# Performance work log

Measured on AMD Instinct MI355X. Metric: run time of the kernel, lower is better.

## Reference

```python
import jax, jax.numpy as jnp
import numpy as np
from jax import lax

B, C, P = 8, 32, 256      # batch, channels, patch side
KB = 2                    # buf_region = kernel_size - stride = 3 - 1
R_MASK = 1                # output_bypassing: last-column patch, r = small_padding = 1


def setup_inputs() -> dict:
    key = jax.random.key(0)
    ks = jax.random.split(key, 5)
    x = jax.random.normal(ks[0], (B, C, P, P), jnp.float32)
    # right-halo stored by the left-neighbor patch (store_right -> last 2 cols)
    rbuf = jax.random.normal(ks[1], (B, C, P, KB), jnp.float32)
    # bottom-halo stored by the top-neighbor patch AFTER its hcat (width P+2)
    bbuf = jax.random.normal(ks[2], (B, C, KB, P + KB), jnp.float32)
    W = jax.random.normal(ks[3], (C, C, 3, 3), jnp.float32) * 0.05
    bias = jax.random.normal(ks[4], (C,), jnp.float32) * 0.05
    return {"x": x, "rbuf": rbuf, "bbuf": bbuf, "W": W, "bias": bias}


def reference(x, rbuf, bbuf, W, bias):
    # output_bypassing: zero the rightmost R_MASK columns (image right edge)
    x = x.at[:, :, :, -R_MASK:].set(0.0)
    # hcat: prepend right-halo from left neighbor -> [B,C,P,P+2]
    x = jnp.concatenate([rbuf, x], axis=-1)
    # vcat: prepend bottom-halo from top neighbor -> [B,C,P+2,P+2]
    x = jnp.concatenate([bbuf, x], axis=-2)
    # (store_bot side effect omitted: pure function returns conv output only)
    out = lax.conv_general_dilated(
        x, W, window_strides=(1, 1), padding='VALID',
        dimension_numbers=('NCHW', 'OIHW', 'NCHW'))  # -> [B,C,P,P]
    return out + bias[None, :, None, None]
```

## Files before the change

kernel.cpp:

```cpp
#include <hip/hip_runtime.h>
#include <cstdint>


constexpr int B  = 8;
constexpr int C  = 32;
constexpr int P  = 256;
constexpr int KB = 2;
constexpr int TH = 16;
constexpr int TW = 32;
constexpr int RS = 36;
constexpr int PL = 652;
constexpr int XSZ = 16 * PL;

typedef short bf16x8 __attribute__((ext_vector_type(8)));
typedef float f32x4  __attribute__((ext_vector_type(4)));
union Frag { uint32_t u[4]; bf16x8 v; };

static __device__ __forceinline__ uint32_t pk_bf16(float lo, float hi) {
    uint32_t a  = __builtin_bit_cast(uint32_t, lo);
    uint32_t b2 = __builtin_bit_cast(uint32_t, hi);
    a  += 0x7FFFu + ((a  >> 16) & 1u);
    b2 += 0x7FFFu + ((b2 >> 16) & 1u);
    return (a >> 16) | (b2 & 0xFFFF0000u);
}

__global__ __launch_bounds__(256) void pack_w_kernel(
    const float* __restrict__ W, uint32_t* __restrict__ wpk)
{
    const int g = blockIdx.x * 256 + threadIdx.x;
    const float4 v = ((const float4*)W)[g];
    const float vv[4] = { v.x, v.y, v.z, v.w };
    uint16_t* wh = (uint16_t*)wpk;
    #pragma unroll
    for (int e = 0; e < 4; ++e) {
        const int flat = 4 * g + e;
        const int t    = flat % 9;
        const int rest = flat / 9;
        const int ic   = rest & 31;
        const int oc   = rest >> 5;
        const uint32_t u = __builtin_bit_cast(uint32_t, vv[e]);
        const uint16_t h = (uint16_t)((u + 0x7FFFu + ((u >> 16) & 1u)) >> 16);
        wh[(t * 512 + oc * 16 + (ic >> 1)) * 2 + (ic & 1)] = h;
    }
}

struct StP {
    float4 a0, a1, c0, c1;
    float  h0l, h0h, h1l, h1h;
};

__global__ __launch_bounds__(256, 3) void conv_mfma(
    const float* __restrict__ x,
    const float* __restrict__ rbuf,
    const float* __restrict__ bbuf,
    const uint32_t* __restrict__ wpk,
    const float* __restrict__ bias,
    float* __restrict__ out)
{
    const int tid  = threadIdx.x;
    const int lane = tid & 63;
    const int w    = tid >> 6;
    const int q    = lane >> 4;
    const int n16  = lane & 15;

    const int swz = (blockIdx.x & 7) * 128 + (blockIdx.x >> 3);
    const int cx = swz & 7, ty = (swz >> 3) & 15, b = swz >> 7;
    const int x0 = cx * TW, y0 = ty * TH;

    __shared__ uint32_t Xs[XSZ];

    const int srow = lane >> 2;
    const int scol = (lane & 3) * 8;
    const bool zc  = (x0 == P - TW) && ((lane & 3) == 3);

    const float* xb = x    + (size_t)b * C * P * P;
    const float* rb = rbuf + (size_t)b * C * P * KB;
    const float* bb = bbuf + (size_t)b * C * KB * (P + KB);
    const float* basep[3] = { xb, rb, bb };
    const int    psz[3]   = { P * P, P * KB, KB * (P + KB) };

    int h_ldso[2], h_ps[2];
    const float* h_bp[2];
    bool h_z[2];
    #pragma unroll
    for (int ci = 0; ci < 2; ++ci) {
        const int c = lane + 64 * ci;
        int prow, pcol;
        if (c < 68) { const int hr = (c >= 34) ? 1 : 0; prow = hr; pcol = c - 34 * hr; }
        else        { const int cc = c - 68; prow = KB + (cc >> 1); pcol = cc & 1; }
        h_ldso[ci] = prow * RS + 2 + pcol;
        const int gr = y0 + prow, gc = x0 + pcol;
        int sel, off; bool z = false;
        if (gr < KB)      { sel = 2; off = gr * (P + KB) + gc; }
        else if (gc < KB) { sel = 1; off = (gr - KB) * KB + gc; }
        else              { sel = 0; off = (gr - KB) * P + (gc - KB); z = (gc == P + KB - 1); }
        h_bp[ci] = basep[sel] + off;
        h_ps[ci] = psz[sel];
        h_z[ci]  = z;
    }
    const bool h1a = lane < 36;

    auto ld = [&](int m, StP& S) {
        const float* pi = xb + (size_t)(2 * m) * (P * P) + (y0 + srow) * P + x0 + scol;
        S.a0 = *(const float4*)pi;
        S.a1 = *(const float4*)(pi + 4);
        S.c0 = *(const float4*)(pi + P * P);
        S.c1 = *(const float4*)(pi + P * P + 4);
        const float* p0 = h_bp[0] + (size_t)(2 * m) * h_ps[0];
        S.h0l = h_z[0] ? 0.f : p0[0];
        S.h0h = h_z[0] ? 0.f : p0[h_ps[0]];
        if (h1a) {
            const float* p1 = h_bp[1] + (size_t)(2 * m) * h_ps[1];
            S.h1l = h_z[1] ? 0.f : p1[0];
            S.h1h = h_z[1] ? 0.f : p1[h_ps[1]];
        }
    };

    auto st = [&](int m, StP& S) {
        float4 a1 = S.a1, c1 = S.c1;
        if (zc) { a1.w = 0.f; c1.w = 0.f; }
        uint4 u0, u1;
        u0.x = pk_bf16(S.a0.x, S.c0.x); u0.y = pk_bf16(S.a0.y, S.c0.y);
        u0.z = pk_bf16(S.a0.z, S.c0.z); u0.w = pk_bf16(S.a0.w, S.c0.w);
        u1.x = pk_bf16(a1.x, c1.x);     u1.y = pk_bf16(a1.y, c1.y);
        u1.z = pk_bf16(a1.z, c1.z);     u1.w = pk_bf16(a1.w, c1.w);
        uint32_t* base = Xs + m * PL + (srow + KB) * RS + 4 + scol;
        *(uint4*)base       = u0;
        *(uint4*)(base + 4) = u1;
        Xs[m * PL + h_ldso[0]] = pk_bf16(S.h0l, S.h0h);
        if (h1a) Xs[m * PL + h_ldso[1]] = pk_bf16(S.h1l, S.h1h);
    };

    const uint4* wp4 = (const uint4*)wpk;
    uint4 wv0 = wp4[tid];
    uint4 wv1 = wp4[256 + tid];
    uint4 wv2 = wp4[512 + tid];
    uint4 wv3 = wp4[768 + tid];
    uint4 wvt;
    const bool wtail = tid < 128;
    if (wtail) wvt = wp4[1024 + tid];
    const float bv0 = bias[n16];
    const float bv1 = bias[16 + n16];

    StP S0, S1, S2, S3;
    ld(w, S0);
    ld(4 + w, S1);

    uint4* xs4 = (uint4*)Xs;
    xs4[tid]       = wv0;
    xs4[256 + tid] = wv1;
    xs4[512 + tid] = wv2;
    xs4[768 + tid] = wv3;
    if (wtail) xs4[1024 + tid] = wvt;
    __syncthreads();

    Frag Bf[9][2];
    #pragma unroll
    for (int t = 0; t < 9; ++t)
        #pragma unroll
        for (int oh = 0; oh < 2; ++oh)
            *(uint4*)Bf[t][oh].u =
                *(const uint4*)&Xs[t * 512 + (oh * 16 + n16) * 16 + q * 4];
    __syncthreads();

    st(w, S0);        ld(8 + w, S2);
    st(4 + w, S1);    ld(12 + w, S3);
    st(8 + w, S2);
    st(12 + w, S3);
    __syncthreads();

    #pragma unroll
    for (int ch = 0; ch < 2; ++ch) {
        f32x4 acc[4][2];
        #pragma unroll
        for (int rr = 0; rr < 4; ++rr)
            #pragma unroll
            for (int oh = 0; oh < 2; ++oh)
                #pragma unroll
                for (int e = 0; e < 4; ++e) acc[rr][oh][e] = 0.f;

        #pragma unroll
        for (int dr = 0; dr < 6; ++dr) {
            Frag A[3];
            const uint32_t* ap = Xs + (4 * q) * PL + (4 * w + dr) * RS + 2 + 16 * ch + n16;
            #pragma unroll
            for (int kx = 0; kx < 3; ++kx)
                #pragma unroll
                for (int p = 0; p < 4; ++p)
                    A[kx].u[p] = ap[p * PL + kx];
            #pragma unroll
            for (int ky = 0; ky < 3; ++ky) {
                const int rr = dr - ky;
                if (rr >= 0 && rr < 4) {
                    #pragma unroll
                    for (int kx = 0; kx < 3; ++kx) {
                        acc[rr][0] = __builtin_amdgcn_mfma_f32_16x16x32_bf16(
                                         A[kx].v, Bf[ky * 3 + kx][0].v, acc[rr][0], 0, 0, 0);
                        acc[rr][1] = __builtin_amdgcn_mfma_f32_16x16x32_bf16(
                                         A[kx].v, Bf[ky * 3 + kx][1].v, acc[rr][1], 0, 0, 0);
                    }
                }
            }
        }

        #pragma unroll
        for (int oh = 0; oh < 2; ++oh) {
            const int oc = oh * 16 + n16;
            const float bv = oh ? bv1 : bv0;
            #pragma unroll
            for (int rr = 0; rr < 4; ++rr) {
                float4 v;
                v.x = acc[rr][oh][0] + bv;
                v.y = acc[rr][oh][1] + bv;
                v.z = acc[rr][oh][2] + bv;
                v.w = acc[rr][oh][3] + bv;
                *(float4*)&out[((size_t)(b * C + oc) * P + (y0 + 4 * w + rr)) * P
                               + x0 + 16 * ch + 4 * q] = v;
            }
        }
    }
}

extern "C" void kernel_launch(void* const* d_in, const int* in_sizes, int n_in,
                              void* d_out, int out_size, void* d_ws, size_t ws_size,
                              hipStream_t stream) {
    const float* x    = (const float*)d_in[0];
    const float* rbuf = (const float*)d_in[1];
    const float* bbuf = (const float*)d_in[2];
    const float* W    = (const float*)d_in[3];
    const float* bias = (const float*)d_in[4];
    float* out = (float*)d_out;
    uint32_t* wpk = (uint32_t*)d_ws;

    pack_w_kernel<<<9, 256, 0, stream>>>(W, wpk);
    conv_mfma<<<1024, 256, 0, stream>>>(x, rbuf, bbuf, wpk, bias, out);
}
```

Measured before the change: 159.8 us.

## Tighten LDS row stride, issue all global loads upfront, target 4 waves per EU

Shrinks the shared-memory row stride from 36 to 34 words and removes the column offset, which changes the LDS bank mapping and slightly reduces footprint. All four input staging loads are now issued before the weight-fragment sync instead of interleaving loads with stores, giving more memory-level parallelism. The LDS stores become 64-bit pairs because 16-byte alignment is lost with the odd offset. The occupancy hint moves from launch_bounds min 3 blocks to waves_per_eu 4, which raises register pressure from the extra staging registers and risks spills.

```diff
diff --git a/kernel.cpp b/kernel.cpp
--- a/kernel.cpp
+++ b/kernel.cpp
@@ -8,8 +8,8 @@
 constexpr int KB = 2;
 constexpr int TH = 16;
 constexpr int TW = 32;
-constexpr int RS = 36;
-constexpr int PL = 652;
+constexpr int RS = 34;
+constexpr int PL = 612;
 constexpr int XSZ = 16 * PL;
 
 typedef short bf16x8 __attribute__((ext_vector_type(8)));
@@ -49,7 +49,10 @@
     float  h0l, h0h, h1l, h1h;
 };
 
-__global__ __launch_bounds__(256, 3) void conv_mfma(
+__global__
+__attribute__((amdgpu_flat_work_group_size(256, 256)))
+__attribute__((amdgpu_waves_per_eu(4, 4)))
+void conv_mfma(
     const float* __restrict__ x,
     const float* __restrict__ rbuf,
     const float* __restrict__ bbuf,
@@ -88,7 +91,7 @@
         int prow, pcol;
         if (c < 68) { const int hr = (c >= 34) ? 1 : 0; prow = hr; pcol = c - 34 * hr; }
         else        { const int cc = c - 68; prow = KB + (cc >> 1); pcol = cc & 1; }
-        h_ldso[ci] = prow * RS + 2 + pcol;
+        h_ldso[ci] = prow * RS + pcol;
         const int gr = y0 + prow, gc = x0 + pcol;
         int sel, off; bool z = false;
         if (gr < KB)      { sel = 2; off = gr * (P + KB) + gc; }
@@ -99,37 +102,6 @@
         h_z[ci]  = z;
     }
     const bool h1a = lane < 36;
-
-    auto ld = [&](int m, StP& S) {
-        const float* pi = xb + (size_t)(2 * m) * (P * P) + (y0 + srow) * P + x0 + scol;
-        S.a0 = *(const float4*)pi;
-        S.a1 = *(const float4*)(pi + 4);
-        S.c0 = *(const float4*)(pi + P * P);
-        S.c1 = *(const float4*)(pi + P * P + 4);
-        const float* p0 = h_bp[0] + (size_t)(2 * m) * h_ps[0];
-        S.h0l = h_z[0] ? 0.f : p0[0];
-        S.h0h = h_z[0] ? 0.f : p0[h_ps[0]];
-        if (h1a) {
-            const float* p1 = h_bp[1] + (size_t)(2 * m) * h_ps[1];
-            S.h1l = h_z[1] ? 0.f : p1[0];
-            S.h1h = h_z[1] ? 0.f : p1[h_ps[1]];
-        }
-    };
-
-    auto st = [&](int m, StP& S) {
-        float4 a1 = S.a1, c1 = S.c1;
-        if (zc) { a1.w = 0.f; c1.w = 0.f; }
-        uint4 u0, u1;
-        u0.x = pk_bf16(S.a0.x, S.c0.x); u0.y = pk_bf16(S.a0.y, S.c0.y);
-        u0.z = pk_bf16(S.a0.z, S.c0.z); u0.w = pk_bf16(S.a0.w, S.c0.w);
-        u1.x = pk_bf16(a1.x, c1.x);     u1.y = pk_bf16(a1.y, c1.y);
-        u1.z = pk_bf16(a1.z, c1.z);     u1.w = pk_bf16(a1.w, c1.w);
-        uint32_t* base = Xs + m * PL + (srow + KB) * RS + 4 + scol;
-        *(uint4*)base       = u0;
-        *(uint4*)(base + 4) = u1;
-        Xs[m * PL + h_ldso[0]] = pk_bf16(S.h0l, S.h0h);
-        if (h1a) Xs[m * PL + h_ldso[1]] = pk_bf16(S.h1l, S.h1h);
-    };
 
     const uint4* wp4 = (const uint4*)wpk;
     uint4 wv0 = wp4[tid];
@@ -142,9 +114,24 @@
     const float bv0 = bias[n16];
     const float bv1 = bias[16 + n16];
 
-    StP S0, S1, S2, S3;
-    ld(w, S0);
-    ld(4 + w, S1);
+    StP S[4];
+    #pragma unroll
+    for (int k2 = 0; k2 < 4; ++k2) {
+        const int m = 4 * k2 + w;
+        const float* pi = xb + (size_t)(2 * m) * (P * P) + (y0 + srow) * P + x0 + scol;
+        S[k2].a0 = *(const float4*)pi;
+        S[k2].a1 = *(const float4*)(pi + 4);
+        S[k2].c0 = *(const float4*)(pi + P * P);
+        S[k2].c1 = *(const float4*)(pi + P * P + 4);
+        const float* p0 = h_bp[0] + (size_t)(2 * m) * h_ps[0];
+        S[k2].h0l = h_z[0] ? 0.f : p0[0];
+        S[k2].h0h = h_z[0] ? 0.f : p0[h_ps[0]];
+        if (h1a) {
+            const float* p1 = h_bp[1] + (size_t)(2 * m) * h_ps[1];
+            S[k2].h1l = h_z[1] ? 0.f : p1[0];
+            S[k2].h1h = h_z[1] ? 0.f : p1[h_ps[1]];
+        }
+    }
 
     uint4* xs4 = (uint4*)Xs;
     xs4[tid]       = wv0;
@@ -163,10 +150,24 @@
                 *(const uint4*)&Xs[t * 512 + (oh * 16 + n16) * 16 + q * 4];
     __syncthreads();
 
-    st(w, S0);        ld(8 + w, S2);
-    st(4 + w, S1);    ld(12 + w, S3);
-    st(8 + w, S2);
-    st(12 + w, S3);
+    #pragma unroll
+    for (int k2 = 0; k2 < 4; ++k2) {
+        const int m = 4 * k2 + w;
+        float4 a1 = S[k2].a1, c1 = S[k2].c1;
+        if (zc) { a1.w = 0.f; c1.w = 0.f; }
+        uint2 p0, p1, p2, p3;
+        p0.x = pk_bf16(S[k2].a0.x, S[k2].c0.x); p0.y = pk_bf16(S[k2].a0.y, S[k2].c0.y);
+        p1.x = pk_bf16(S[k2].a0.z, S[k2].c0.z); p1.y = pk_bf16(S[k2].a0.w, S[k2].c0.w);
+        p2.x = pk_bf16(a1.x, c1.x);             p2.y = pk_bf16(a1.y, c1.y);
+        p3.x = pk_bf16(a1.z, c1.z);             p3.y = pk_bf16(a1.w, c1.w);
+        uint32_t* base = Xs + m * PL + (srow + KB) * RS + KB + scol;
+        *(uint2*)(base + 0) = p0;
+        *(uint2*)(base + 2) = p1;
+        *(uint2*)(base + 4) = p2;
+        *(uint2*)(base + 6) = p3;
+        Xs[m * PL + h_ldso[0]] = pk_bf16(S[k2].h0l, S[k2].h0h);
+        if (h1a) Xs[m * PL + h_ldso[1]] = pk_bf16(S[k2].h1l, S[k2].h1h);
+    }
     __syncthreads();
 
     #pragma unroll
@@ -182,7 +183,7 @@
         #pragma unroll
         for (int dr = 0; dr < 6; ++dr) {
             Frag A[3];
-            const uint32_t* ap = Xs + (4 * q) * PL + (4 * w + dr) * RS + 2 + 16 * ch + n16;
+            const uint32_t* ap = Xs + (4 * q) * PL + (4 * w + dr) * RS + 16 * ch + n16;
             #pragma unroll
             for (int kx = 0; kx < 3; ++kx)
                 #pragma unroll
```

Result: slower. 223.1 us (+39.7%).
